# Optimization experiments

Measured on AMD Instinct MI355X. Metric: run time of the kernel, lower is better.

The kernel has to match this reference:

```python
import jax, jax.numpy as jnp
import numpy as np

K = 20
SLOPE = 0.2


def _edge_conv(x, params):
    """DynamicEdgeConv: kNN graph on x, edge MLP on [x_i, x_j - x_i], max-aggregate.

    x: [B, N, D] -> [B, N, D_out]
    """
    sq = jnp.sum(x * x, axis=-1)  # [B, N]
    # squared euclidean distances [B, N, N]
    d = sq[:, :, None] + sq[:, None, :] - 2.0 * jnp.einsum('bnd,bmd->bnm', x, x)
    _, idx = jax.lax.top_k(-d, K)  # [B, N, K] nearest (incl. self, dist 0)
    xj = jax.vmap(lambda xb, ib: xb[ib])(x, idx)  # [B, N, K, D]
    xi = x[:, :, None, :]
    h = jnp.concatenate([jnp.broadcast_to(xi, xj.shape), xj - xi], axis=-1)  # [B,N,K,2D]
    for W, b in params:
        h = jax.nn.leaky_relu(h @ W + b, SLOPE)
    return jnp.max(h, axis=2)  # max aggregation over neighbors


def setup_inputs() -> dict:
    key = jax.random.key(0)
    ks = jax.random.split(key, 10)
    B, N = 8, 4096
    H = 64
    def lin(k, fi, fo):
        return jax.random.normal(k, (fi, fo), jnp.float32) * (1.0 / np.sqrt(fi))
    inp = {
        'pos': jax.random.normal(ks[0], (B, N, 3), jnp.float32),
        'w11': lin(ks[1], 6, H),   'b11': jnp.zeros((H,), jnp.float32),
        'w12': lin(ks[2], H, H),   'b12': jnp.zeros((H,), jnp.float32),
        'w13': lin(ks[3], H, H),   'b13': jnp.zeros((H,), jnp.float32),
        'w21': lin(ks[4], 2 * H, H), 'b21': jnp.zeros((H,), jnp.float32),
        'w22': lin(ks[5], H, H),   'b22': jnp.zeros((H,), jnp.float32),
        'w23': lin(ks[6], H, H),   'b23': jnp.zeros((H,), jnp.float32),
        'w31': lin(ks[7], 2 * H, H), 'b31': jnp.zeros((H,), jnp.float32),
        'w32': lin(ks[8], H, H),   'b32': jnp.zeros((H,), jnp.float32),
        'w33': lin(ks[9], H, H),   'b33': jnp.zeros((H,), jnp.float32),
    }
    return inp


def reference(pos, w11, b11, w12, b12, w13, b13,
              w21, b21, w22, b22, w23, b23,
              w31, b31, w32, b32, w33, b33):
    x = _edge_conv(pos, [(w11, b11), (w12, b12), (w13, b13)])
    x = _edge_conv(x, [(w21, b21), (w22, b22), (w23, b23)])
    x = _edge_conv(x, [(w31, b31), (w32, b32), (w33, b33)])
    return x
```

## Files before the change

kernel.cpp:

```cpp
#include <hip/hip_runtime.h>
#include <stdint.h>

#define BATCH 8
#define NPTS 4096
#define KNN 20
#define TILE 64
#define NTILES (NPTS / TILE)
#define BTHR 256
#define CAP 4
#define CAPMAX 8
constexpr float SLOPE = 0.2f;

typedef unsigned long long u64;
#define INIT_KEY 0xFF7FFFFFFFFFFFFFULL

template<int D>
__global__ __launch_bounds__(256) void sq_kernel(const float* __restrict__ X,
                                                 float* __restrict__ sq) {
    const int i = blockIdx.x * 256 + threadIdx.x;
    if constexpr (D == 3) {
        const float* p = X + (size_t)i * 3;
        sq[i] = p[0] * p[0] + p[1] * p[1] + p[2] * p[2];
    } else {
        const float4* p = (const float4*)(X + (size_t)i * 64);
        float s = 0.f;
        #pragma unroll
        for (int k = 0; k < 16; ++k) {
            float4 v = p[k];
            s += v.x * v.x; s += v.y * v.y; s += v.z * v.z; s += v.w * v.w;
        }
        sq[i] = s;
    }
}

__device__ __forceinline__ u64 pack_key(float d, unsigned j) {
    unsigned ub = __float_as_uint(d);
    ub = (ub & 0x80000000u) ? ~ub : (ub | 0x80000000u);
    return ((u64)ub << 32) | j;
}
__device__ __forceinline__ float key_hi_to_d(unsigned hi) {
    unsigned u = (hi & 0x80000000u) ? (hi ^ 0x80000000u) : ~hi;
    return __uint_as_float(u);
}
__device__ __forceinline__ void insert_key(u64 (&lst)[KNN], u64 c) {
    #pragma unroll
    for (int k = 0; k < KNN; ++k) {
        const u64 lo = (lst[k] < c) ? lst[k] : c;
        const u64 hi = (lst[k] < c) ? c : lst[k];
        lst[k] = lo; c = hi;
    }
}
__device__ __forceinline__ void flush_buf(u64 (&lst)[KNN], const u64* __restrict__ buf,
                                          int t, int& cnt, float& tmax) {
    for (int i = 0; i < CAPMAX; ++i) {
        if (i < cnt) {
            const u64 key = buf[i * BTHR + t];
            if (key < lst[KNN - 1]) insert_key(lst, key);
        }
    }
    cnt = 0;
    tmax = key_hi_to_d((unsigned)(lst[KNN - 1] >> 32));
}

template<int D>
__global__ __launch_bounds__(BTHR) void knn3_kernel(
    const float* __restrict__ X, const float* __restrict__ sq,
    int* __restrict__ knn_idx)
{
    __shared__ alignas(16) float smem[17280];
    float* xq   = smem;
    float* xj   = smem + 4352;
    float* dist = smem + 8704;
    float* sqq  = smem + 13056;
    float* sqj  = smem + 13120;
    u64*   buf  = (u64*)(smem + 13184);
    u64*   lists = (u64*)smem;

    const int t = threadIdx.x;
    const int b = blockIdx.y;
    const int qbase = blockIdx.x * 64;
    const float* Xb  = X  + (size_t)b * NPTS * D;
    const float* sqb = sq + (size_t)b * NPTS;

    const int qg = t >> 4, jg = t & 15;
    const int q  = t >> 2, s  = t & 3;

    float4 aq[(D == 3) ? 4 : 1];
    float sqq_r[4];
    if constexpr (D == 3) {
        #pragma unroll
        for (int rr = 0; rr < 4; ++rr) {
            const float* qp = Xb + (size_t)(qbase + 4 * qg + rr) * 3;
            aq[rr].x = qp[0]; aq[rr].y = qp[1]; aq[rr].z = qp[2]; aq[rr].w = 0.f;
            sqq_r[rr] = sqb[qbase + 4 * qg + rr];
        }
        if (t < 64) {
            const float* row = Xb + (size_t)t * 3;
            xj[0 * 68 + t] = row[0];
            xj[1 * 68 + t] = row[1];
            xj[2 * 68 + t] = row[2];
            sqj[t] = sqb[t];
        }
    } else {
        #pragma unroll
        for (int ci = t; ci < 1024; ci += BTHR) {
            const int r = ci >> 4, c4 = ci & 15;
            *(float4*)&xq[r * 68 + 4 * c4] =
                *(const float4*)&Xb[(size_t)(qbase + r) * 64 + 4 * c4];
        }
        #pragma unroll
        for (int ci = t; ci < 1024; ci += BTHR) {
            const int r = ci >> 4, c4 = ci & 15;
            const int c4s = (c4 + (r >> 2)) & 15;
            *(float4*)&xj[r * 68 + 4 * c4s] =
                *(const float4*)&Xb[(size_t)r * 64 + 4 * c4];
        }
        if (t < 64) { sqq[t] = sqb[qbase + t]; sqj[t] = sqb[t]; }
    }
    __syncthreads();
    if constexpr (D != 3) {
        #pragma unroll
        for (int rr = 0; rr < 4; ++rr) sqq_r[rr] = sqq[4 * qg + rr];
    }

    u64 lst[KNN];
    #pragma unroll
    for (int k = 0; k < KNN; ++k) lst[k] = INIT_KEY;
    float tmax = 3.402823466e38f;
    int cnt = 0;

    for (int tile = 0; tile < NTILES; ++tile) {
        if constexpr (D == 3) {
            float sj[4];
            #pragma unroll
            for (int cc = 0; cc < 4; ++cc) sj[cc] = sqj[4 * jg + cc];
            float4 bx, by, bz;
            bx.x = xj[0 * 68 + 4 * jg + 0]; bx.y = xj[0 * 68 + 4 * jg + 1];
            bx.z = xj[0 * 68 + 4 * jg + 2]; bx.w = xj[0 * 68 + 4 * jg + 3];
            by.x = xj[1 * 68 + 4 * jg + 0]; by.y = xj[1 * 68 + 4 * jg + 1];
            by.z = xj[1 * 68 + 4 * jg + 2]; by.w = xj[1 * 68 + 4 * jg + 3];
            bz.x = xj[2 * 68 + 4 * jg + 0]; bz.y = xj[2 * 68 + 4 * jg + 1];
            bz.z = xj[2 * 68 + 4 * jg + 2]; bz.w = xj[2 * 68 + 4 * jg + 3];
            #pragma unroll
            for (int rr = 0; rr < 4; ++rr) {
                float4 dv;
                dv.x = sqq_r[rr] + sj[0] - 2.f * (aq[rr].x * bx.x + aq[rr].y * by.x + aq[rr].z * bz.x);
                dv.y = sqq_r[rr] + sj[1] - 2.f * (aq[rr].x * bx.y + aq[rr].y * by.y + aq[rr].z * bz.y);
                dv.z = sqq_r[rr] + sj[2] - 2.f * (aq[rr].x * bx.z + aq[rr].y * by.z + aq[rr].z * bz.z);
                dv.w = sqq_r[rr] + sj[3] - 2.f * (aq[rr].x * bx.w + aq[rr].y * by.w + aq[rr].z * bz.w);
                *(float4*)&dist[(4 * qg + rr) * 68 + 4 * jg] = dv;
            }
        } else {
            float acc[4][4];
            #pragma unroll
            for (int rr = 0; rr < 4; ++rr)
                #pragma unroll
                for (int cc = 0; cc < 4; ++cc) acc[rr][cc] = 0.f;
            #pragma unroll
            for (int k = 0; k < 16; ++k) {
                float4 a[4], bv[4];
                #pragma unroll
                for (int rr = 0; rr < 4; ++rr)
                    a[rr] = *(const float4*)&xq[(4 * qg + rr) * 68 + 4 * k];
                const int kx = (k + jg) & 15;
                #pragma unroll
                for (int cc = 0; cc < 4; ++cc)
                    bv[cc] = *(const float4*)&xj[(4 * jg + cc) * 68 + 4 * kx];
                #pragma unroll
                for (int rr = 0; rr < 4; ++rr)
                    #pragma unroll
                    for (int cc = 0; cc < 4; ++cc) {
                        float v = acc[rr][cc];
                        v = fmaf(a[rr].x, bv[cc].x, v);
                        v = fmaf(a[rr].y, bv[cc].y, v);
                        v = fmaf(a[rr].z, bv[cc].z, v);
                        v = fmaf(a[rr].w, bv[cc].w, v);
                        acc[rr][cc] = v;
                    }
            }
            float sj[4];
            #pragma unroll
            for (int cc = 0; cc < 4; ++cc) sj[cc] = sqj[4 * jg + cc];
            #pragma unroll
            for (int rr = 0; rr < 4; ++rr) {
                float4 dv;
                dv.x = sqq_r[rr] + sj[0] - 2.f * acc[rr][0];
                dv.y = sqq_r[rr] + sj[1] - 2.f * acc[rr][1];
                dv.z = sqq_r[rr] + sj[2] - 2.f * acc[rr][2];
                dv.w = sqq_r[rr] + sj[3] - 2.f * acc[rr][3];
                *(float4*)&dist[(4 * qg + rr) * 68 + 4 * jg] = dv;
            }
        }
        __syncthreads();

        if (tile + 1 < NTILES) {
            const int cb = (tile + 1) * TILE;
            if constexpr (D == 3) {
                if (t < 64) {
                    const float* row = Xb + (size_t)(cb + t) * 3;
                    xj[0 * 68 + t] = row[0];
                    xj[1 * 68 + t] = row[1];
                    xj[2 * 68 + t] = row[2];
                    sqj[t] = sqb[cb + t];
                }
            } else {
                #pragma unroll
                for (int ci = t; ci < 1024; ci += BTHR) {
                    const int r = ci >> 4, c4 = ci & 15;
                    const int c4s = (c4 + (r >> 2)) & 15;
                    *(float4*)&xj[r * 68 + 4 * c4s] =
                        *(const float4*)&Xb[(size_t)(cb + r) * 64 + 4 * c4];
                }
                if (t < 64) sqj[t] = sqb[cb + t];
            }
        }

        {
            const int cbase = tile * TILE;
            const float* drow = &dist[q * 68 + s * 16];
            #pragma unroll
            for (int g = 0; g < 4; ++g) {
                const float4 dv = *(const float4*)&drow[g * 4];
                const float dd0 = dv.x, dd1 = dv.y, dd2 = dv.z, dd3 = dv.w;
                if (dd0 <= tmax) { buf[cnt * BTHR + t] = pack_key(dd0, cbase + s * 16 + g * 4 + 0); ++cnt; }
                if (dd1 <= tmax) { buf[cnt * BTHR + t] = pack_key(dd1, cbase + s * 16 + g * 4 + 1); ++cnt; }
                if (dd2 <= tmax) { buf[cnt * BTHR + t] = pack_key(dd2, cbase + s * 16 + g * 4 + 2); ++cnt; }
                if (dd3 <= tmax) { buf[cnt * BTHR + t] = pack_key(dd3, cbase + s * 16 + g * 4 + 3); ++cnt; }
                if (__any(cnt >= CAP)) flush_buf(lst, buf, t, cnt, tmax);
            }
        }
        __syncthreads();
    }
    if (__any(cnt > 0)) flush_buf(lst, buf, t, cnt, tmax);

    #pragma unroll
    for (int k = 0; k < KNN; ++k) lists[t * KNN + k] = lst[k];
    __syncthreads();

    if (t < 64) {
        const u64* L0 = lists + (size_t)(t * 4 + 0) * KNN;
        const u64* L1 = L0 + KNN;
        const u64* L2 = L1 + KNN;
        const u64* L3 = L2 + KNN;
        int p0 = 0, p1 = 0, p2 = 0, p3 = 0;
        int* outp = knn_idx + ((size_t)b * NPTS + qbase + t) * KNN;
        for (int k = 0; k < KNN; ++k) {
            const u64 h0 = L0[p0], h1 = L1[p1], h2 = L2[p2], h3 = L3[p3];
            const u64 m01 = (h0 < h1) ? h0 : h1;
            const u64 m23 = (h2 < h3) ? h2 : h3;
            const u64 m   = (m01 < m23) ? m01 : m23;
            outp[k] = (int)(unsigned)(m & 0xffffffffu);
            if (m == h0) ++p0; else if (m == h1) ++p1; else if (m == h2) ++p2; else ++p3;
        }
    }
}

template<int D>
__global__ __launch_bounds__(256) void uc_kernel(
    const float* __restrict__ X, const float* __restrict__ W1,
    const float* __restrict__ b1, float* __restrict__ u, float* __restrict__ cvec) {
    __shared__ float Xs[16 * D];
    const int n0 = blockIdx.x * 16;
    const int t = threadIdx.x;
    for (int i = t; i < 16 * D; i += 256)
        Xs[i] = X[(size_t)n0 * D + i];
    __syncthreads();

    const int o = t & 63;
    const int pg = t >> 6;
    float va[4] = {0.f, 0.f, 0.f, 0.f};
    float vb[4] = {0.f, 0.f, 0.f, 0.f};
    for (int d = 0; d < D; ++d) {
        const float wa = W1[d * 64 + o];
        const float wb = W1[(D + d) * 64 + o];
        #pragma unroll
        for (int pi = 0; pi < 4; ++pi) {
            const float x = Xs[(pg * 4 + pi) * D + d];
            va[pi] += x * wa;
            vb[pi] += x * wb;
        }
    }
    const float bo = b1[o];
    #pragma unroll
    for (int pi = 0; pi < 4; ++pi) {
        const size_t n = (size_t)n0 + pg * 4 + pi;
        u[n * 64 + o] = vb[pi];
        cvec[n * 64 + o] = va[pi] - vb[pi] + bo;
    }
}

__device__ __forceinline__ void gemm_acc(const float* __restrict__ Xs,
                                         const float* __restrict__ Ws,
                                         const float* __restrict__ bias,
                                         float (&acc)[5][4], const int t) {
    const int rg = t >> 4, og = t & 15;
    #pragma unroll
    for (int oc = 0; oc < 4; ++oc) {
        const float bb = bias[4 * og + oc];
        #pragma unroll
        for (int rr = 0; rr < 5; ++rr) acc[rr][oc] = bb;
    }
    #pragma unroll
    for (int k4 = 0; k4 < 16; ++k4) {
        float4 xv[5];
        #pragma unroll
        for (int rr = 0; rr < 5; ++rr)
            xv[rr] = *(const float4*)&Xs[(5 * rg + rr) * 68 + 4 * k4];
        float4 wv[4];
        #pragma unroll
        for (int kk = 0; kk < 4; ++kk)
            wv[kk] = *(const float4*)&Ws[(4 * k4 + kk) * 64 + 4 * og];
        #pragma unroll
        for (int rr = 0; rr < 5; ++rr) {
            acc[rr][0] += xv[rr].x * wv[0].x + xv[rr].y * wv[1].x + xv[rr].z * wv[2].x + xv[rr].w * wv[3].x;
            acc[rr][1] += xv[rr].x * wv[0].y + xv[rr].y * wv[1].y + xv[rr].z * wv[2].y + xv[rr].w * wv[3].y;
            acc[rr][2] += xv[rr].x * wv[0].z + xv[rr].y * wv[1].z + xv[rr].z * wv[2].z + xv[rr].w * wv[3].z;
            acc[rr][3] += xv[rr].x * wv[0].w + xv[rr].y * wv[1].w + xv[rr].z * wv[2].w + xv[rr].w * wv[3].w;
        }
    }
}

__global__ __launch_bounds__(256) void edge_kernel(
    const float* __restrict__ u, const float* __restrict__ cvec,
    const int* __restrict__ knn_idx,
    const float* __restrict__ W2, const float* __restrict__ b2,
    const float* __restrict__ W3, const float* __restrict__ b3,
    float* __restrict__ out) {
    __shared__ alignas(16) float h1s[80 * 68];
    __shared__ alignas(16) float Ws[64 * 64];
    __shared__ float cs[256];
    __shared__ float mxs[16 * 64];
    __shared__ int idxs[80];

    const int t = threadIdx.x;
    const int p0 = blockIdx.x * 4;
    const int b = p0 >> 12;

    cs[t] = cvec[(size_t)p0 * 64 + t];
    if (t < 80) idxs[t] = knn_idx[(size_t)p0 * KNN + t];
    for (int i = t; i < 4096; i += 256) Ws[i] = W2[i];
    __syncthreads();

    {
        const int wave = t >> 6, lane = t & 63;
        for (int e = wave; e < 80; e += 4) {
            const int j = idxs[e];
            const float val = u[((size_t)(b << 12) + j) * 64 + lane];
            const float pre = cs[(e / 20) * 64 + lane] + val;
            h1s[e * 68 + lane] = (pre > 0.f) ? pre : SLOPE * pre;
        }
    }
    __syncthreads();

    float acc[5][4];
    gemm_acc(h1s, Ws, b2, acc, t);
    __syncthreads();

    {
        const int rg = t >> 4, og = t & 15;
        #pragma unroll
        for (int rr = 0; rr < 5; ++rr)
            #pragma unroll
            for (int oc = 0; oc < 4; ++oc) {
                float v = acc[rr][oc];
                v = (v > 0.f) ? v : SLOPE * v;
                h1s[(5 * rg + rr) * 68 + 4 * og + oc] = v;
            }
        for (int i = t; i < 4096; i += 256) Ws[i] = W3[i];
    }
    __syncthreads();

    gemm_acc(h1s, Ws, b3, acc, t);
    {
        const int rg = t >> 4, og = t & 15;
        #pragma unroll
        for (int oc = 0; oc < 4; ++oc) {
            float m = -1e30f;
            #pragma unroll
            for (int rr = 0; rr < 5; ++rr) {
                float v = acc[rr][oc];
                v = (v > 0.f) ? v : SLOPE * v;
                m = fmaxf(m, v);
            }
            mxs[rg * 64 + 4 * og + oc] = m;
        }
    }
    __syncthreads();

    const int p = t >> 6, col = t & 63;
    const float m = fmaxf(fmaxf(mxs[(4 * p + 0) * 64 + col], mxs[(4 * p + 1) * 64 + col]),
                          fmaxf(mxs[(4 * p + 2) * 64 + col], mxs[(4 * p + 3) * 64 + col]));
    out[(size_t)(p0 + p) * 64 + col] = m;
}

extern "C" void kernel_launch(void* const* d_in, const int* in_sizes, int n_in,
                              void* d_out, int out_size, void* d_ws, size_t ws_size,
                              hipStream_t stream) {
    const float* pos = (const float*)d_in[0];
    const float* w11 = (const float*)d_in[1];  const float* b11 = (const float*)d_in[2];
    const float* w12 = (const float*)d_in[3];  const float* b12 = (const float*)d_in[4];
    const float* w13 = (const float*)d_in[5];  const float* b13 = (const float*)d_in[6];
    const float* w21 = (const float*)d_in[7];  const float* b21 = (const float*)d_in[8];
    const float* w22 = (const float*)d_in[9];  const float* b22 = (const float*)d_in[10];
    const float* w23 = (const float*)d_in[11]; const float* b23 = (const float*)d_in[12];
    const float* w31 = (const float*)d_in[13]; const float* b31 = (const float*)d_in[14];
    const float* w32 = (const float*)d_in[15]; const float* b32 = (const float*)d_in[16];
    const float* w33 = (const float*)d_in[17]; const float* b33 = (const float*)d_in[18];

    const int BN = BATCH * NPTS;
    float* ws = (float*)d_ws;
    float* sqb = ws;
    int*   idx = (int*)(sqb + BN);
    float* x1  = (float*)(idx + (size_t)BN * KNN);
    float* ubuf = x1 + (size_t)BN * 64;
    float* cbuf = ubuf + (size_t)BN * 64;
    float* x2  = cbuf + (size_t)BN * 64;

    const dim3 knn_grid(NPTS / 64, BATCH);

    sq_kernel<3><<<BN / 256, 256, 0, stream>>>(pos, sqb);
    knn3_kernel<3><<<knn_grid, BTHR, 0, stream>>>(pos, sqb, idx);
    uc_kernel<3><<<BN / 16, 256, 0, stream>>>(pos, w11, b11, ubuf, cbuf);
    edge_kernel<<<BN / 4, 256, 0, stream>>>(ubuf, cbuf, idx, w12, b12, w13, b13, x1);

    sq_kernel<64><<<BN / 256, 256, 0, stream>>>(x1, sqb);
    knn3_kernel<64><<<knn_grid, BTHR, 0, stream>>>(x1, sqb, idx);
    uc_kernel<64><<<BN / 16, 256, 0, stream>>>(x1, w21, b21, ubuf, cbuf);
    edge_kernel<<<BN / 4, 256, 0, stream>>>(ubuf, cbuf, idx, w22, b22, w23, b23, x2);

    sq_kernel<64><<<BN / 256, 256, 0, stream>>>(x2, sqb);
    knn3_kernel<64><<<knn_grid, BTHR, 0, stream>>>(x2, sqb, idx);
    uc_kernel<64><<<BN / 16, 256, 0, stream>>>(x2, w31, b31, ubuf, cbuf);
    edge_kernel<<<BN / 4, 256, 0, stream>>>(ubuf, cbuf, idx, w32, b32, w33, b33, (float*)d_out);
}
```

Baseline: 2.617 ms.

## Prefetch next kNN tile into registers before distance compute; enlarge candidate buffer

The kNN kernel now issues the global loads for the next candidate tile into registers at the top of each iteration, before the distance computation. After the barrier it writes those registers to shared memory, so global latency overlaps with the compute instead of sitting on the critical path. It also raises the candidate buffer capacity (CAP 4 to 6, CAPMAX 8 to 10) and grows shared memory to match, so list-insertion flushes happen less often. The cost is extra registers for the prefetch and more LDS per block, which may reduce occupancy.

```diff
diff --git a/kernel.cpp b/kernel.cpp
--- a/kernel.cpp
+++ b/kernel.cpp
@@ -7,8 +7,8 @@
 #define TILE 64
 #define NTILES (NPTS / TILE)
 #define BTHR 256
-#define CAP 4
-#define CAPMAX 8
+#define CAP 6
+#define CAPMAX 10
 constexpr float SLOPE = 0.2f;
 
 typedef unsigned long long u64;
@@ -67,7 +67,7 @@
     const float* __restrict__ X, const float* __restrict__ sq,
     int* __restrict__ knn_idx)
 {
-    __shared__ alignas(16) float smem[17280];
+    __shared__ alignas(16) float smem[18304];
     float* xq   = smem;
     float* xj   = smem + 4352;
     float* dist = smem + 8704;
@@ -129,7 +129,30 @@
     float tmax = 3.402823466e38f;
     int cnt = 0;
 
+    float4 preg[(D == 3) ? 1 : 4];
+    float  sprg = 0.f;
+
     for (int tile = 0; tile < NTILES; ++tile) {
+        const bool has_next = (tile + 1 < NTILES);
+        if (has_next) {
+            const int cb = (tile + 1) * TILE;
+            if constexpr (D == 3) {
+                if (t < 64) {
+                    const float* row = Xb + (size_t)(cb + t) * 3;
+                    preg[0].x = row[0]; preg[0].y = row[1]; preg[0].z = row[2];
+                    sprg = sqb[cb + t];
+                }
+            } else {
+                #pragma unroll
+                for (int i = 0; i < 4; ++i) {
+                    const int ci = i * BTHR + t;
+                    const int r = ci >> 4, c4 = ci & 15;
+                    preg[i] = *(const float4*)&Xb[(size_t)(cb + r) * 64 + 4 * c4];
+                }
+                if (t < 64) sprg = sqb[cb + t];
+            }
+        }
+
         if constexpr (D == 3) {
             float sj[4];
             #pragma unroll
@@ -193,25 +216,23 @@
         }
         __syncthreads();
 
-        if (tile + 1 < NTILES) {
-            const int cb = (tile + 1) * TILE;
+        if (has_next) {
             if constexpr (D == 3) {
                 if (t < 64) {
-                    const float* row = Xb + (size_t)(cb + t) * 3;
-                    xj[0 * 68 + t] = row[0];
-                    xj[1 * 68 + t] = row[1];
-                    xj[2 * 68 + t] = row[2];
-                    sqj[t] = sqb[cb + t];
+                    xj[0 * 68 + t] = preg[0].x;
+                    xj[1 * 68 + t] = preg[0].y;
+                    xj[2 * 68 + t] = preg[0].z;
+                    sqj[t] = sprg;
                 }
             } else {
                 #pragma unroll
-                for (int ci = t; ci < 1024; ci += BTHR) {
+                for (int i = 0; i < 4; ++i) {
+                    const int ci = i * BTHR + t;
                     const int r = ci >> 4, c4 = ci & 15;
                     const int c4s = (c4 + (r >> 2)) & 15;
-                    *(float4*)&xj[r * 68 + 4 * c4s] =
-                        *(const float4*)&Xb[(size_t)(cb + r) * 64 + 4 * c4];
+                    *(float4*)&xj[r * 68 + 4 * c4s] = preg[i];
                 }
-                if (t < 64) sqj[t] = sqb[cb + t];
+                if (t < 64) sqj[t] = sprg;
             }
         }
 
```

After: 2.641 ms. About the same (+0.9%).
